# Optimization experiments

Measured on AMD Instinct MI355X. Metric: run time of the kernel, lower is better.

## Reference

```python
import jax, jax.numpy as jnp
import numpy as np
import math

B, SQ, SKV, H = 8, 1024, 1024, 1024
NH, HD = 16, 64  # num_attention_heads, attention_head_size


def setup_inputs() -> dict:
    key = jax.random.key(0)
    ks = jax.random.split(key, 6)
    s = 1.0 / math.sqrt(H)
    return {
        "hidden_states": jax.random.normal(ks[0], (B, SQ, H), jnp.float32),
        "keyvalue_states": jax.random.normal(ks[1], (B, SKV, H), jnp.float32),
        "attention_mask": jnp.zeros((B, 1, 1, SKV), jnp.float32),
        "Wq": jax.random.normal(ks[2], (H, H), jnp.float32) * s,
        "bq": jnp.zeros((H,), jnp.float32),
        "Wk": jax.random.normal(ks[3], (H, H), jnp.float32) * s,
        "bk": jnp.zeros((H,), jnp.float32),
        "Wv": jax.random.normal(ks[4], (H, H), jnp.float32) * s,
        "bv": jnp.zeros((H,), jnp.float32),
    }


def _split_heads(x):
    # [B, S, H] -> [B, NH, S, HD]
    b, s, _ = x.shape
    return x.reshape(b, s, NH, HD).transpose(0, 2, 1, 3)


def reference(hidden_states, keyvalue_states, attention_mask, Wq, bq, Wk, bk, Wv, bv):
    q = _split_heads(hidden_states @ Wq.T + bq)     # [B, NH, SQ, HD]
    k = _split_heads(keyvalue_states @ Wk.T + bk)   # [B, NH, SKV, HD]
    v = _split_heads(keyvalue_states @ Wv.T + bv)   # [B, NH, SKV, HD]
    scores = jnp.einsum("bhqd,bhkd->bhqk", q, k) / math.sqrt(HD)
    scores = scores + attention_mask                 # additive mask broadcast
    probs = jax.nn.softmax(scores, axis=-1)          # dropout = identity (eval)
    ctx = jnp.einsum("bhqk,bhkd->bhqd", probs, v)
    ctx = ctx.transpose(0, 2, 1, 3).reshape(hidden_states.shape[0], -1, NH * HD)
    return ctx
```

## Files before the change

### kernel.cpp

```cpp
#include <hip/hip_runtime.h>
#include <hip/hip_bf16.h>


typedef __attribute__((ext_vector_type(8))) short short8;
typedef __attribute__((ext_vector_type(4))) short short4v;
typedef __attribute__((ext_vector_type(4))) float f32x4;

#define AS1(p) ((const __attribute__((address_space(1))) void*)(p))
#define AS3(p) ((__attribute__((address_space(3))) void*)(p))

__device__ inline short f2bs(float x) {
    __hip_bfloat16 h = __float2bfloat16(x);
    return *reinterpret_cast<short*>(&h);
}

__global__ __launch_bounds__(256) void cvt_bf16(
    const float* __restrict__ s0, const float* __restrict__ s1,
    const float* __restrict__ s2, const float* __restrict__ s3,
    const float* __restrict__ s4,
    short* __restrict__ d0, short* __restrict__ d1,
    short* __restrict__ d2, short* __restrict__ d3, short* __restrict__ d4)
{
    const float* s; short* d; int n4;
    switch (blockIdx.y) {
        case 0: s = s0; d = d0; n4 = 2097152; break;
        case 1: s = s1; d = d1; n4 = 2097152; break;
        case 2: s = s2; d = d2; n4 = 262144;  break;
        case 3: s = s3; d = d3; n4 = 262144;  break;
        default: s = s4; d = d4; n4 = 262144; break;
    }
    for (int i = blockIdx.x * 256 + threadIdx.x; i < n4; i += gridDim.x * 256) {
        float4 v = ((const float4*)s)[i];
        short4v o;
        o.x = f2bs(v.x); o.y = f2bs(v.y); o.z = f2bs(v.z); o.w = f2bs(v.w);
        ((short4v*)d)[i] = o;
    }
}

__global__ __launch_bounds__(256) void qkv_gemm(
    const short* __restrict__ hsb, const short* __restrict__ kvb,
    const short* __restrict__ wqb, const short* __restrict__ wkb,
    const short* __restrict__ wvb,
    const float* __restrict__ bq, const float* __restrict__ bk,
    const float* __restrict__ bv,
    short* __restrict__ qo, short* __restrict__ ko, short* __restrict__ vo)
{
    const short* A; const short* W; const float* bias; short* dst;
    int z = blockIdx.z;
    if (z == 0)      { A = hsb; W = wqb; bias = bq; dst = qo; }
    else if (z == 1) { A = kvb; W = wkb; bias = bk; dst = ko; }
    else             { A = kvb; W = wvb; bias = bv; dst = vo; }

    __shared__ __align__(16) short As[128 * 64];
    __shared__ __align__(16) short Bs[128 * 64];

    const int t = threadIdx.x;
    const int lane = t & 63;
    const int wave = t >> 6;
    const int lane15 = lane & 15;
    const int quad = lane >> 4;
    const int wm = (wave & 1) * 64;
    const int wn = (wave >> 1) * 64;
    const int m0 = blockIdx.x * 128;
    const int n0 = blockIdx.y * 128;

    f32x4 acc[4][4] = {};

    for (int k0 = 0; k0 < 1024; k0 += 64) {
        #pragma unroll
        for (int i = 0; i < 4; ++i) {
            int c = i * 256 + t;
            int row = c >> 3;
            int gc = (c & 7) ^ (row & 7);
            __builtin_amdgcn_global_load_lds(
                AS1(&A[(size_t)(m0 + row) * 1024 + k0 + gc * 8]), AS3(&As[c * 8]), 16, 0, 0);
            __builtin_amdgcn_global_load_lds(
                AS1(&W[(size_t)(n0 + row) * 1024 + k0 + gc * 8]), AS3(&Bs[c * 8]), 16, 0, 0);
        }
        __syncthreads();

        #pragma unroll
        for (int kc = 0; kc < 2; ++kc) {
            short8 af[4], bf[4];
            #pragma unroll
            for (int i = 0; i < 4; ++i) {
                int rr = wm + i * 16 + lane15;
                af[i] = *(short8*)&As[rr * 64 + (((kc * 4 + quad)) ^ (rr & 7)) * 8];
            }
            #pragma unroll
            for (int i = 0; i < 4; ++i) {
                int rn = wn + i * 16 + lane15;
                bf[i] = *(short8*)&Bs[rn * 64 + (((kc * 4 + quad)) ^ (rn & 7)) * 8];
            }
            #pragma unroll
            for (int mi = 0; mi < 4; ++mi)
                #pragma unroll
                for (int ni = 0; ni < 4; ++ni)
                    acc[mi][ni] = __builtin_amdgcn_mfma_f32_16x16x32_bf16(
                        af[mi], bf[ni], acc[mi][ni], 0, 0, 0);
        }
        __syncthreads();
    }

    if (z != 2) {
        #pragma unroll
        for (int ni = 0; ni < 4; ++ni) {
            int col = n0 + wn + ni * 16 + lane15;
            float bb = bias[col];
            int h = col >> 6, d = col & 63;
            #pragma unroll
            for (int mi = 0; mi < 4; ++mi) {
                int m = m0 + wm + mi * 16 + quad * 4;
                int b = m >> 10, s = m & 1023;
                size_t base = (size_t)((b * 16 + h) * 1024 + s) * 64 + d;
                #pragma unroll
                for (int r = 0; r < 4; ++r)
                    dst[base + (size_t)r * 64] = f2bs(acc[mi][ni][r] + bb);
            }
        }
    } else {
        #pragma unroll
        for (int ni = 0; ni < 4; ++ni) {
            int col = n0 + wn + ni * 16 + lane15;
            float bb = bias[col];
            int h = col >> 6, d = col & 63;
            #pragma unroll
            for (int mi = 0; mi < 4; ++mi) {
                int m = m0 + wm + mi * 16 + quad * 4;
                int b = m >> 10, s = m & 1023;
                short4v pk;
                pk.x = f2bs(acc[mi][ni][0] + bb);
                pk.y = f2bs(acc[mi][ni][1] + bb);
                pk.z = f2bs(acc[mi][ni][2] + bb);
                pk.w = f2bs(acc[mi][ni][3] + bb);
                *(short4v*)&dst[(size_t)((b * 16 + h) * 64 + d) * 1024 + s] = pk;
            }
        }
    }
}

#define LDP 66
#define EXPC 0.18033688011112042f
__global__ __launch_bounds__(256, 2) void attn(
    const short* __restrict__ q, const short* __restrict__ k,
    const short* __restrict__ vt, const float* __restrict__ mask,
    float* __restrict__ out)
{
    __shared__ __align__(16) short Ks[2][64 * 64];
    __shared__ __align__(16) short Vs[2][64 * 64];
    __shared__ __align__(16) short Ps[128 * LDP];
    __shared__ __align__(16) short Ms[1024];

    const int t = threadIdx.x;
    const int lane = t & 63;
    const int wq = t >> 6;
    const int lane15 = lane & 15;
    const int quad = lane >> 4;
    const int qt = blockIdx.x, h = blockIdx.y, b = blockIdx.z;
    const int bh = b * 16 + h;

    const short* qbase = q + (size_t)(bh * 1024 + qt * 128) * 64;
    const short* kbase = k + (size_t)bh * 1024 * 64;
    const short* vbase = vt + (size_t)bh * 64 * 1024;

    {
        float4 mv = ((const float4*)(mask + b * 1024))[t];
        short4v msv;
        msv.x = f2bs(mv.x * 1.4426950408889634f);
        msv.y = f2bs(mv.y * 1.4426950408889634f);
        msv.z = f2bs(mv.z * 1.4426950408889634f);
        msv.w = f2bs(mv.w * 1.4426950408889634f);
        *(short4v*)&Ms[t * 4] = msv;
    }

    short8 qf[2][2];
    #pragma unroll
    for (int nt = 0; nt < 2; ++nt)
        #pragma unroll
        for (int kc = 0; kc < 2; ++kc)
            qf[nt][kc] = *(const short8*)&qbase[
                (size_t)(wq * 32 + nt * 16 + lane15) * 64 + kc * 32 + quad * 8];

    #pragma unroll
    for (int i = 0; i < 2; ++i) {
        int c = i * 256 + t;
        int row = c >> 3;
        int gc = (c & 7) ^ (row & 7);
        __builtin_amdgcn_global_load_lds(AS1(kbase + (size_t)row * 64 + gc * 8),
                                         AS3(&Ks[0][c * 8]), 16, 0, 0);
        __builtin_amdgcn_global_load_lds(AS1(vbase + (size_t)row * 1024 + gc * 8),
                                         AS3(&Vs[0][c * 8]), 16, 0, 0);
    }

    f32x4 o_acc[2][4] = {};
    float l_sum[2] = {0.f, 0.f};

    for (int kt = 0; kt < 16; ++kt) {
        __syncthreads();
        if (kt < 15) {
            int kv1 = (kt + 1) * 64;
            int nb = (kt + 1) & 1;
            #pragma unroll
            for (int i = 0; i < 2; ++i) {
                int c = i * 256 + t;
                int row = c >> 3;
                int gc = (c & 7) ^ (row & 7);
                __builtin_amdgcn_global_load_lds(
                    AS1(kbase + (size_t)(kv1 + row) * 64 + gc * 8),
                    AS3(&Ks[nb][c * 8]), 16, 0, 0);
                __builtin_amdgcn_global_load_lds(
                    AS1(vbase + (size_t)row * 1024 + kv1 + gc * 8),
                    AS3(&Vs[nb][c * 8]), 16, 0, 0);
            }
        }
        const short* ks_ = Ks[kt & 1];
        const short* vs_ = Vs[kt & 1];

        f32x4 s_acc[2][4] = {};
        #pragma unroll
        for (int kc = 0; kc < 2; ++kc) {
            short8 afk[4];
            #pragma unroll
            for (int mt = 0; mt < 4; ++mt) {
                int rr = mt * 16 + lane15;
                afk[mt] = *(short8*)&ks_[rr * 64 + (((kc * 4 + quad)) ^ (rr & 7)) * 8];
            }
            #pragma unroll
            for (int nt = 0; nt < 2; ++nt)
                #pragma unroll
                for (int mt = 0; mt < 4; ++mt)
                    s_acc[nt][mt] = __builtin_amdgcn_mfma_f32_16x16x32_bf16(
                        afk[mt], qf[nt][kc], s_acc[nt][mt], 0, 0, 0);
        }

        float mr[4][4];
        #pragma unroll
        for (int mt = 0; mt < 4; ++mt) {
            int2 mw = *(int2*)&Ms[kt * 64 + mt * 16 + quad * 4];
            mr[mt][0] = __uint_as_float(((unsigned)mw.x) << 16);
            mr[mt][1] = __uint_as_float(((unsigned)mw.x) & 0xffff0000u);
            mr[mt][2] = __uint_as_float(((unsigned)mw.y) << 16);
            mr[mt][3] = __uint_as_float(((unsigned)mw.y) & 0xffff0000u);
        }

        #pragma unroll
        for (int nt = 0; nt < 2; ++nt) {
            float rsum = 0.f;
            #pragma unroll
            for (int mt = 0; mt < 4; ++mt) {
                float p0 = exp2f(s_acc[nt][mt][0] * EXPC + mr[mt][0]);
                float p1 = exp2f(s_acc[nt][mt][1] * EXPC + mr[mt][1]);
                float p2 = exp2f(s_acc[nt][mt][2] * EXPC + mr[mt][2]);
                float p3 = exp2f(s_acc[nt][mt][3] * EXPC + mr[mt][3]);
                rsum += (p0 + p1) + (p2 + p3);
                short4v pk;
                pk.x = f2bs(p0); pk.y = f2bs(p1); pk.z = f2bs(p2); pk.w = f2bs(p3);
                *(short4v*)&Ps[(wq * 32 + nt * 16 + lane15) * LDP + mt * 16 + quad * 4] = pk;
            }
            rsum += __shfl_xor(rsum, 16, 64);
            rsum += __shfl_xor(rsum, 32, 64);
            l_sum[nt] += rsum;
        }

        #pragma unroll
        for (int kc = 0; kc < 2; ++kc) {
            short8 afp[2], bfv[4];
            #pragma unroll
            for (int mt = 0; mt < 2; ++mt)
                afp[mt] = *(short8*)&Ps[(wq * 32 + mt * 16 + lane15) * LDP + kc * 32 + quad * 8];
            #pragma unroll
            for (int nt = 0; nt < 4; ++nt) {
                int rv = nt * 16 + lane15;
                bfv[nt] = *(short8*)&vs_[rv * 64 + (((kc * 4 + quad)) ^ (rv & 7)) * 8];
            }
            #pragma unroll
            for (int mt = 0; mt < 2; ++mt)
                #pragma unroll
                for (int nt = 0; nt < 4; ++nt)
                    o_acc[mt][nt] = __builtin_amdgcn_mfma_f32_16x16x32_bf16(
                        afp[mt], bfv[nt], o_acc[mt][nt], 0, 0, 0);
        }
    }

    #pragma unroll
    for (int mt = 0; mt < 2; ++mt) {
        #pragma unroll
        for (int r = 0; r < 4; ++r) {
            float lv = __shfl(l_sum[mt], quad * 4 + r, 64);
            float inv = 1.f / lv;
            int qrow = qt * 128 + wq * 32 + mt * 16 + quad * 4 + r;
            size_t base = (size_t)(b * 1024 + qrow) * 1024 + h * 64;
            #pragma unroll
            for (int nt = 0; nt < 4; ++nt)
                out[base + nt * 16 + lane15] = o_acc[mt][nt][r] * inv;
        }
    }
}

extern "C" void kernel_launch(void* const* d_in, const int* in_sizes, int n_in,
                              void* d_out, int out_size, void* d_ws, size_t ws_size,
                              hipStream_t stream) {
    const float* hs   = (const float*)d_in[0];
    const float* kvs  = (const float*)d_in[1];
    const float* mask = (const float*)d_in[2];
    const float* Wq   = (const float*)d_in[3];
    const float* bq   = (const float*)d_in[4];
    const float* Wk   = (const float*)d_in[5];
    const float* bk   = (const float*)d_in[6];
    const float* Wv   = (const float*)d_in[7];
    const float* bv   = (const float*)d_in[8];
    float* outp = (float*)d_out;

    const size_t big = (size_t)8 * 1024 * 1024;
    const size_t wsz = (size_t)1024 * 1024;
    short* q_ws  = (short*)d_ws;
    short* k_ws  = q_ws  + big;
    short* vt_ws = k_ws  + big;
    short* hsb   = vt_ws + big;
    short* kvb   = hsb   + big;
    short* wqb   = kvb   + big;
    short* wkb   = wqb   + wsz;
    short* wvb   = wkb   + wsz;

    cvt_bf16<<<dim3(1024, 5), 256, 0, stream>>>(hs, kvs, Wq, Wk, Wv,
                                                hsb, kvb, wqb, wkb, wvb);
    qkv_gemm<<<dim3(64, 8, 3), 256, 0, stream>>>(hsb, kvb, wqb, wkb, wvb,
                                                 bq, bk, bv, q_ws, k_ws, vt_ws);
    attn<<<dim3(8, 16, 8), 256, 0, stream>>>(q_ws, k_ws, vt_ws, mask, outp);
}
```

Baseline: 261.3 us.

## Switch GEMM and attention to 32x32x16 MFMA tiles with remapped grid

Replaces 16x16x32 bf16 MFMAs with 32x32x16 MFMAs in both the QKV projection GEMM and the attention kernel, which halves the number of fragment loads per FLOP and simplifies row-sum reductions to a single cross-half shuffle. The attention kernel also drops the bf16 mask staging in LDS and reads the mask directly from global memory, and computes the probability sum from the bf16-rounded values using manual rounding and perm packing. It flattens the grid to 1D with a block-id mapping that groups query tiles of neighbouring heads, changes the P padding, and removes the occupancy hint. Larger accumulators raise register pressure and may lower occupancy.

```diff
diff --git a/kernel.cpp b/kernel.cpp
--- a/kernel.cpp
+++ b/kernel.cpp
@@ -5,6 +5,7 @@
 typedef __attribute__((ext_vector_type(8))) short short8;
 typedef __attribute__((ext_vector_type(4))) short short4v;
 typedef __attribute__((ext_vector_type(4))) float f32x4;
+typedef __attribute__((ext_vector_type(16))) float f32x16;
 
 #define AS1(p) ((const __attribute__((address_space(1))) void*)(p))
 #define AS3(p) ((__attribute__((address_space(3))) void*)(p))
@@ -57,14 +58,14 @@
     const int t = threadIdx.x;
     const int lane = t & 63;
     const int wave = t >> 6;
-    const int lane15 = lane & 15;
-    const int quad = lane >> 4;
+    const int lane31 = lane & 31;
+    const int hi = lane >> 5;
     const int wm = (wave & 1) * 64;
     const int wn = (wave >> 1) * 64;
     const int m0 = blockIdx.x * 128;
     const int n0 = blockIdx.y * 128;
 
-    f32x4 acc[4][4] = {};
+    f32x16 acc[2][2] = {};
 
     for (int k0 = 0; k0 < 1024; k0 += 64) {
         #pragma unroll
@@ -80,68 +81,75 @@
         __syncthreads();
 
         #pragma unroll
-        for (int kc = 0; kc < 2; ++kc) {
-            short8 af[4], bf[4];
-            #pragma unroll
-            for (int i = 0; i < 4; ++i) {
-                int rr = wm + i * 16 + lane15;
-                af[i] = *(short8*)&As[rr * 64 + (((kc * 4 + quad)) ^ (rr & 7)) * 8];
-            }
-            #pragma unroll
-            for (int i = 0; i < 4; ++i) {
-                int rn = wn + i * 16 + lane15;
-                bf[i] = *(short8*)&Bs[rn * 64 + (((kc * 4 + quad)) ^ (rn & 7)) * 8];
-            }
-            #pragma unroll
-            for (int mi = 0; mi < 4; ++mi)
+        for (int kc = 0; kc < 4; ++kc) {
+            short8 af[2], bf[2];
+            #pragma unroll
+            for (int mt = 0; mt < 2; ++mt) {
+                int rr = wm + mt * 32 + lane31;
+                af[mt] = *(short8*)&As[rr * 64 + ((kc * 2 + hi) ^ (rr & 7)) * 8];
+            }
+            #pragma unroll
+            for (int nt = 0; nt < 2; ++nt) {
+                int rn = wn + nt * 32 + lane31;
+                bf[nt] = *(short8*)&Bs[rn * 64 + ((kc * 2 + hi) ^ (rn & 7)) * 8];
+            }
+            #pragma unroll
+            for (int mt = 0; mt < 2; ++mt)
                 #pragma unroll
-                for (int ni = 0; ni < 4; ++ni)
-                    acc[mi][ni] = __builtin_amdgcn_mfma_f32_16x16x32_bf16(
-                        af[mi], bf[ni], acc[mi][ni], 0, 0, 0);
+                for (int nt = 0; nt < 2; ++nt)
+                    acc[mt][nt] = __builtin_amdgcn_mfma_f32_32x32x16_bf16(
+                        af[mt], bf[nt], acc[mt][nt], 0, 0, 0);
         }
         __syncthreads();
     }
 
     if (z != 2) {
         #pragma unroll
-        for (int ni = 0; ni < 4; ++ni) {
-            int col = n0 + wn + ni * 16 + lane15;
+        for (int nt = 0; nt < 2; ++nt) {
+            int col = n0 + wn + nt * 32 + lane31;
             float bb = bias[col];
             int h = col >> 6, d = col & 63;
             #pragma unroll
-            for (int mi = 0; mi < 4; ++mi) {
-                int m = m0 + wm + mi * 16 + quad * 4;
-                int b = m >> 10, s = m & 1023;
-                size_t base = (size_t)((b * 16 + h) * 1024 + s) * 64 + d;
+            for (int mt = 0; mt < 2; ++mt) {
                 #pragma unroll
-                for (int r = 0; r < 4; ++r)
-                    dst[base + (size_t)r * 64] = f2bs(acc[mi][ni][r] + bb);
+                for (int rg = 0; rg < 4; ++rg) {
+                    int m = m0 + wm + mt * 32 + rg * 8 + hi * 4;
+                    int b = m >> 10, s = m & 1023;
+                    size_t base = (size_t)((b * 16 + h) * 1024 + s) * 64 + d;
+                    #pragma unroll
+                    for (int r = 0; r < 4; ++r)
+                        dst[base + (size_t)r * 64] = f2bs(acc[mt][nt][rg * 4 + r] + bb);
+                }
             }
         }
     } else {
         #pragma unroll
-        for (int ni = 0; ni < 4; ++ni) {
-            int col = n0 + wn + ni * 16 + lane15;
+        for (int nt = 0; nt < 2; ++nt) {
+            int col = n0 + wn + nt * 32 + lane31;
             float bb = bias[col];
             int h = col >> 6, d = col & 63;
             #pragma unroll
-            for (int mi = 0; mi < 4; ++mi) {
-                int m = m0 + wm + mi * 16 + quad * 4;
-                int b = m >> 10, s = m & 1023;
-                short4v pk;
-                pk.x = f2bs(acc[mi][ni][0] + bb);
-                pk.y = f2bs(acc[mi][ni][1] + bb);
-                pk.z = f2bs(acc[mi][ni][2] + bb);
-                pk.w = f2bs(acc[mi][ni][3] + bb);
-                *(short4v*)&dst[(size_t)((b * 16 + h) * 64 + d) * 1024 + s] = pk;
-            }
-        }
-    }
-}
-
-#define LDP 66
+            for (int mt = 0; mt < 2; ++mt) {
+                #pragma unroll
+                for (int rg = 0; rg < 4; ++rg) {
+                    int m = m0 + wm + mt * 32 + rg * 8 + hi * 4;
+                    int b = m >> 10, s = m & 1023;
+                    short4v pk;
+                    pk.x = f2bs(acc[mt][nt][rg * 4 + 0] + bb);
+                    pk.y = f2bs(acc[mt][nt][rg * 4 + 1] + bb);
+                    pk.z = f2bs(acc[mt][nt][rg * 4 + 2] + bb);
+                    pk.w = f2bs(acc[mt][nt][rg * 4 + 3] + bb);
+                    *(short4v*)&dst[(size_t)((b * 16 + h) * 64 + d) * 1024 + s] = pk;
+                }
+            }
+        }
+    }
+}
+
+#define LDP 72
 #define EXPC 0.18033688011112042f
-__global__ __launch_bounds__(256, 2) void attn(
+#define LOG2E 1.4426950408889634f
+__global__ __launch_bounds__(256) void attn(
     const short* __restrict__ q, const short* __restrict__ k,
     const short* __restrict__ vt, const float* __restrict__ mask,
     float* __restrict__ out)
@@ -149,37 +157,27 @@
     __shared__ __align__(16) short Ks[2][64 * 64];
     __shared__ __align__(16) short Vs[2][64 * 64];
     __shared__ __align__(16) short Ps[128 * LDP];
-    __shared__ __align__(16) short Ms[1024];
 
     const int t = threadIdx.x;
     const int lane = t & 63;
     const int wq = t >> 6;
-    const int lane15 = lane & 15;
-    const int quad = lane >> 4;
-    const int qt = blockIdx.x, h = blockIdx.y, b = blockIdx.z;
-    const int bh = b * 16 + h;
+    const int lane31 = lane & 31;
+    const int hi = lane >> 5;
+
+    const int id = blockIdx.x;
+    const int bh = (id >> 6) * 8 + (id & 7);
+    const int qt = (id >> 3) & 7;
+    const int b = bh >> 4, h = bh & 15;
 
     const short* qbase = q + (size_t)(bh * 1024 + qt * 128) * 64;
     const short* kbase = k + (size_t)bh * 1024 * 64;
     const short* vbase = vt + (size_t)bh * 64 * 1024;
-
-    {
-        float4 mv = ((const float4*)(mask + b * 1024))[t];
-        short4v msv;
-        msv.x = f2bs(mv.x * 1.4426950408889634f);
-        msv.y = f2bs(mv.y * 1.4426950408889634f);
-        msv.z = f2bs(mv.z * 1.4426950408889634f);
-        msv.w = f2bs(mv.w * 1.4426950408889634f);
-        *(short4v*)&Ms[t * 4] = msv;
-    }
-
-    short8 qf[2][2];
+    const float* mbase = mask + b * 1024;
+
+    short8 qf[4];
     #pragma unroll
-    for (int nt = 0; nt < 2; ++nt)
-        #pragma unroll
-        for (int kc = 0; kc < 2; ++kc)
-            qf[nt][kc] = *(const short8*)&qbase[
-                (size_t)(wq * 32 + nt * 16 + lane15) * 64 + kc * 32 + quad * 8];
+    for (int kc = 0; kc < 4; ++kc)
+        qf[kc] = *(const short8*)&qbase[(size_t)(wq * 32 + lane31) * 64 + kc * 16 + hi * 8];
 
     #pragma unroll
     for (int i = 0; i < 2; ++i) {
@@ -192,8 +190,8 @@
                                          AS3(&Vs[0][c * 8]), 16, 0, 0);
     }
 
-    f32x4 o_acc[2][4] = {};
-    float l_sum[2] = {0.f, 0.f};
+    f32x16 o_acc[2] = {};
+    float l_sum = 0.f;
 
     for (int kt = 0; kt < 16; ++kt) {
         __syncthreads();
@@ -215,84 +213,64 @@
         }
         const short* ks_ = Ks[kt & 1];
         const short* vs_ = Vs[kt & 1];
-
-        f32x4 s_acc[2][4] = {};
-        #pragma unroll
-        for (int kc = 0; kc < 2; ++kc) {
-            short8 afk[4];
-            #pragma unroll
-            for (int mt = 0; mt < 4; ++mt) {
-                int rr = mt * 16 + lane15;
-                afk[mt] = *(short8*)&ks_[rr * 64 + (((kc * 4 + quad)) ^ (rr & 7)) * 8];
-            }
+        const int kv0 = kt * 64;
+
+        f32x16 sacc[2] = {};
+        #pragma unroll
+        for (int kc = 0; kc < 4; ++kc) {
+            #pragma unroll
+            for (int mt = 0; mt < 2; ++mt) {
+                int rr = mt * 32 + lane31;
+                short8 ak = *(short8*)&ks_[rr * 64 + ((kc * 2 + hi) ^ (rr & 7)) * 8];
+                sacc[mt] = __builtin_amdgcn_mfma_f32_32x32x16_bf16(ak, qf[kc], sacc[mt], 0, 0, 0);
+            }
+        }
+
+        #pragma unroll
+        for (int mt = 0; mt < 2; ++mt) {
+            #pragma unroll
+            for (int rg = 0; rg < 4; ++rg) {
+                int kvl = mt * 32 + rg * 8 + hi * 4;
+                f32x4 mk = *(const f32x4*)&mbase[kv0 + kvl];
+                unsigned u0 = __float_as_uint(exp2f(sacc[mt][rg*4+0] * EXPC + mk[0] * LOG2E)) + 0x8000u;
+                unsigned u1 = __float_as_uint(exp2f(sacc[mt][rg*4+1] * EXPC + mk[1] * LOG2E)) + 0x8000u;
+                unsigned u2 = __float_as_uint(exp2f(sacc[mt][rg*4+2] * EXPC + mk[2] * LOG2E)) + 0x8000u;
+                unsigned u3 = __float_as_uint(exp2f(sacc[mt][rg*4+3] * EXPC + mk[3] * LOG2E)) + 0x8000u;
+                l_sum += (__uint_as_float(u0 & 0xffff0000u) + __uint_as_float(u1 & 0xffff0000u))
+                       + (__uint_as_float(u2 & 0xffff0000u) + __uint_as_float(u3 & 0xffff0000u));
+                int2 pk;
+                pk.x = (int)__builtin_amdgcn_perm(u1, u0, 0x07060302u);
+                pk.y = (int)__builtin_amdgcn_perm(u3, u2, 0x07060302u);
+                *(int2*)&Ps[(wq * 32 + lane31) * LDP + kvl] = pk;
+            }
+        }
+
+        #pragma unroll
+        for (int kc = 0; kc < 4; ++kc) {
+            short8 ap = *(short8*)&Ps[(wq * 32 + lane31) * LDP + kc * 16 + hi * 8];
+            #pragma unroll
+            for (int nt = 0; nt < 2; ++nt) {
+                int rv = nt * 32 + lane31;
+                short8 bv_ = *(short8*)&vs_[rv * 64 + ((kc * 2 + hi) ^ (rv & 7)) * 8];
+                o_acc[nt] = __builtin_amdgcn_mfma_f32_32x32x16_bf16(ap, bv_, o_acc[nt], 0, 0, 0);
+            }
+        }
+    }
+
+    l_sum += __shfl_xor(l_sum, 32, 64);
+    float invl = 1.f / l_sum;
+
+    #pragma unroll
+    for (int rg = 0; rg < 4; ++rg) {
+        #pragma unroll
+        for (int r = 0; r < 4; ++r) {
+            int qrow_l = rg * 8 + hi * 4 + r;
+            float lv = __shfl(invl, qrow_l, 64);
+            int qrow = qt * 128 + wq * 32 + qrow_l;
+            size_t base = (size_t)(b * 1024 + qrow) * 1024 + h * 64;
             #pragma unroll
             for (int nt = 0; nt < 2; ++nt)
-                #pragma unroll
-                for (int mt = 0; mt < 4; ++mt)
-                    s_acc[nt][mt] = __builtin_amdgcn_mfma_f32_16x16x32_bf16(
-                        afk[mt], qf[nt][kc], s_acc[nt][mt], 0, 0, 0);
-        }
-
-        float mr[4][4];
-        #pragma unroll
-        for (int mt = 0; mt < 4; ++mt) {
-            int2 mw = *(int2*)&Ms[kt * 64 + mt * 16 + quad * 4];
-            mr[mt][0] = __uint_as_float(((unsigned)mw.x) << 16);
-            mr[mt][1] = __uint_as_float(((unsigned)mw.x) & 0xffff0000u);
-            mr[mt][2] = __uint_as_float(((unsigned)mw.y) << 16);
-            mr[mt][3] = __uint_as_float(((unsigned)mw.y) & 0xffff0000u);
-        }
-
-        #pragma unroll
-        for (int nt = 0; nt < 2; ++nt) {
-            float rsum = 0.f;
-            #pragma unroll
-            for (int mt = 0; mt < 4; ++mt) {
-                float p0 = exp2f(s_acc[nt][mt][0] * EXPC + mr[mt][0]);
-                float p1 = exp2f(s_acc[nt][mt][1] * EXPC + mr[mt][1]);
-                float p2 = exp2f(s_acc[nt][mt][2] * EXPC + mr[mt][2]);
-                float p3 = exp2f(s_acc[nt][mt][3] * EXPC + mr[mt][3]);
-                rsum += (p0 + p1) + (p2 + p3);
-                short4v pk;
-                pk.x = f2bs(p0); pk.y = f2bs(p1); pk.z = f2bs(p2); pk.w = f2bs(p3);
-                *(short4v*)&Ps[(wq * 32 + nt * 16 + lane15) * LDP + mt * 16 + quad * 4] = pk;
-            }
-            rsum += __shfl_xor(rsum, 16, 64);
-            rsum += __shfl_xor(rsum, 32, 64);
-            l_sum[nt] += rsum;
-        }
-
-        #pragma unroll
-        for (int kc = 0; kc < 2; ++kc) {
-            short8 afp[2], bfv[4];
-            #pragma unroll
-            for (int mt = 0; mt < 2; ++mt)
-                afp[mt] = *(short8*)&Ps[(wq * 32 + mt * 16 + lane15) * LDP + kc * 32 + quad * 8];
-            #pragma unroll
-            for (int nt = 0; nt < 4; ++nt) {
-                int rv = nt * 16 + lane15;
-                bfv[nt] = *(short8*)&vs_[rv * 64 + (((kc * 4 + quad)) ^ (rv & 7)) * 8];
-            }
-            #pragma unroll
-            for (int mt = 0; mt < 2; ++mt)
-                #pragma unroll
-                for (int nt = 0; nt < 4; ++nt)
-                    o_acc[mt][nt] = __builtin_amdgcn_mfma_f32_16x16x32_bf16(
-                        afp[mt], bfv[nt], o_acc[mt][nt], 0, 0, 0);
-        }
-    }
-
-    #pragma unroll
-    for (int mt = 0; mt < 2; ++mt) {
-        #pragma unroll
-        for (int r = 0; r < 4; ++r) {
-            float lv = __shfl(l_sum[mt], quad * 4 + r, 64);
-            float inv = 1.f / lv;
-            int qrow = qt * 128 + wq * 32 + mt * 16 + quad * 4 + r;
-            size_t base = (size_t)(b * 1024 + qrow) * 1024 + h * 64;
-            #pragma unroll
-            for (int nt = 0; nt < 4; ++nt)
-                out[base + nt * 16 + lane15] = o_acc[mt][nt][r] * inv;
+                out[base + nt * 32 + lane31] = o_acc[nt][rg * 4 + r] * lv;
         }
     }
 }
@@ -326,5 +304,5 @@
                                                 hsb, kvb, wqb, wkb, wvb);
     qkv_gemm<<<dim3(64, 8, 3), 256, 0, stream>>>(hsb, kvb, wqb, wkb, wvb,
                                                  bq, bk, bv, q_ws, k_ws, vt_ws);
-    attn<<<dim3(8, 16, 8), 256, 0, stream>>>(q_ws, k_ws, vt_ws, mask, outp);
-}
+    attn<<<dim3(1024), 256, 0, stream>>>(q_ws, k_ws, vt_ws, mask, outp);
+}
```

Result: slower. 294.5 us (+12.7%).
